# Performance work log

Hardware: AMD Instinct MI355X
Metric: run time of the kernel (lower is better)

## Reference

```python
import jax, jax.numpy as jnp
import numpy as np
from jax import lax

DIM = 1024
NUM_HEADS = 16
B, L = 4, 4096


def setup_inputs() -> dict:
    key = jax.random.key(0)
    ks = jax.random.split(key, 7)
    D = DIM // NUM_HEADS
    s = lambda fan_in: 1.0 / np.sqrt(fan_in)
    x = jax.random.normal(ks[0], (B, L, DIM), dtype=jnp.float32)
    w_qk = jax.random.uniform(ks[1], (2 * DIM, DIM), jnp.float32, -s(DIM), s(DIM))
    b_qk = jax.random.uniform(ks[2], (2 * DIM,), jnp.float32, -s(DIM), s(DIM))
    w_v = jax.random.uniform(ks[3], (DIM, DIM), jnp.float32, -s(DIM), s(DIM))
    b_v = jax.random.uniform(ks[4], (DIM,), jnp.float32, -s(DIM), s(DIM))
    # depthwise Conv1d: out_channels=D, in_channels/groups=1, kernel=3
    w_lepe = jax.random.uniform(ks[5], (D, 1, 3), jnp.float32, -s(3), s(3))
    b_lepe = jax.random.uniform(ks[6], (D,), jnp.float32, -s(3), s(3))
    return {"x": x, "w_qk": w_qk, "b_qk": b_qk, "w_v": w_v, "b_v": b_v,
            "w_lepe": w_lepe, "b_lepe": b_lepe, "num_heads": NUM_HEADS}


def _lepe_add(a, w_lepe, b_lepe):
    # a: (B,H,L,D). Faithful to torch: raw reshape (NOT transpose) to (B*H, D, L),
    # depthwise conv over last axis, reshape back to (B,H,D,L), then transpose.
    Bc, H, Lc, D = a.shape
    ar = a.reshape(Bc * H, D, Lc)
    conv = lax.conv_general_dilated(
        ar, w_lepe, window_strides=(1,), padding=((1, 1),),
        feature_group_count=D,
        dimension_numbers=("NCH", "OIH", "NCH"))
    conv = conv + b_lepe[None, :, None]
    return a + conv.reshape(Bc, H, D, Lc).transpose(0, 1, 3, 2)


def reference(x, w_qk, b_qk, w_v, b_v, w_lepe, b_lepe, num_heads):
    Bc, Lc, C = x.shape
    H = num_heads
    D = C // H
    qk = (x @ w_qk.T + b_qk).reshape(Bc, Lc, 2, H, D).transpose(2, 0, 3, 1, 4)
    q, k = qk[0], qk[1]                                  # (B,H,L,D)
    v = (x @ w_v.T + b_v).reshape(Bc, Lc, H, D).transpose(0, 2, 1, 3)
    q = jax.nn.elu(q) + 1.0
    k = jax.nn.elu(k) + 1.0
    q = _lepe_add(q, w_lepe, b_lepe)
    k = _lepe_add(k, w_lepe, b_lepe)
    k_mean = k.mean(axis=2, keepdims=True)               # (B,H,1,D)
    z = 1.0 / (jnp.einsum("bhld,bhmd->bhlm", q, k_mean) + 1e-6)  # (B,H,L,1)
    kv = jnp.einsum("bhld,bhle->bhde", k, v) / Lc        # (B,H,D,D)
    out = jnp.einsum("bhld,bhde->bhle", q, kv) * z       # (B,H,L,D)
    return out.transpose(0, 2, 1, 3).reshape(Bc, Lc, C)
```

## Files before the change

kernel.cpp:

```cpp
#include <hip/hip_runtime.h>
#include <hip/hip_bf16.h>
#include <stdint.h>

typedef __bf16 bf16;
typedef __bf16 bf16x8 __attribute__((ext_vector_type(8)));
typedef __bf16 bf16x4 __attribute__((ext_vector_type(4)));
typedef float  f32x4  __attribute__((ext_vector_type(4)));

static __device__ __forceinline__ void gll16(const void* g, void* l) {
    __builtin_amdgcn_global_load_lds((__attribute__((address_space(1))) void*)(void*)g,
                                     (__attribute__((address_space(3))) void*)l, 16, 0, 0);
}

__global__ __launch_bounds__(256) void cvt_f32_bf16(const float* __restrict__ in,
                                                    bf16* __restrict__ out, int n4) {
    int i = blockIdx.x * 256 + threadIdx.x;
    const int stride = gridDim.x * 256;
    for (; i < n4; i += stride) {
        f32x4 v = *(const f32x4*)(in + (size_t)i * 4);
        bf16x4 o;
        o[0] = (bf16)v[0]; o[1] = (bf16)v[1]; o[2] = (bf16)v[2]; o[3] = (bf16)v[3];
        *(bf16x4*)(out + (size_t)i * 4) = o;
    }
}

#define WAITV(n) asm volatile("s_waitcnt vmcnt(" #n ")" ::: "memory")
#define STA(s_, half, pass, k0_) \
    gll16(Xs + (size_t)((half) * 128 + (pass) * 64) * 1024 + (k0_), \
          lds + (s_) * 32768 + (half) * 16384 + (pass) * 8192 + t * 16)
#define STB(s_, half, pass, k0_) \
    gll16(Ws + (size_t)((half) * 128 + (pass) * 64) * 1024 + (k0_), \
          lds + 65536 + (s_) * 32768 + (half) * 16384 + (pass) * 8192 + t * 16)

__global__ __launch_bounds__(512, 2) void gemm_qkv(const bf16* __restrict__ X,
                                                   const bf16* __restrict__ W,
                                                   const float* __restrict__ b_qk,
                                                   const float* __restrict__ b_v,
                                                   bf16* __restrict__ Y) {
    __shared__ char lds[131072];
    const int t    = threadIdx.x;
    const int lane = t & 63;
    const int wid  = t >> 6;
    const int wm   = wid >> 2, wn = wid & 3;

    const int bid = blockIdx.x;
    const int wg  = (bid & 7) * 96 + (bid >> 3);
    const int m0  = (wg & 63) * 256;
    const int n0  = (wg >> 6) * 256;

    const int scol = (((t & 7) ^ ((t >> 3) & 7)) * 8);
    const bf16* Xs = X + (size_t)(m0 + (t >> 3)) * 1024 + scol;
    const bf16* Ws = W + (size_t)(n0 + (t >> 3)) * 1024 + scol;

    const int fr = lane & 15;
    const int l7 = lane & 7;
    const int ax0 = (((lane >> 4) + 0) ^ l7) << 4;
    const int ax1 = (((lane >> 4) + 4) ^ l7) << 4;
    const int baseA = wm * 16384 + fr * 128;
    const int baseB = 65536 + (wn >> 1) * 16384 + ((wn & 1) * 64 + fr) * 128;

    f32x4 acc[8][4] = {};
    bf16x8 bF[4][2];

    STB(0, 0, 0, 0); STB(0, 0, 1, 0); STB(0, 1, 0, 0); STB(0, 1, 1, 0);
    STA(0, 0, 0, 0); STA(0, 1, 0, 0); STA(0, 0, 1, 0); STA(0, 1, 1, 0);
    WAITV(2);
    __builtin_amdgcn_s_barrier();

    for (int j = 0; j < 16; ++j) {
        const int s  = j & 1;
        const int sn = s ^ 1;
        const int kn = (j + 1) << 6;
        const bool st = j < 15;
        const int sA = s * 32768 + baseA;
        const int sB = s * 32768 + baseB;

#pragma unroll
        for (int q = 0; q < 4; ++q) {
            bf16x8 aF[2][2];
#pragma unroll
            for (int m2 = 0; m2 < 2; ++m2) {
                aF[m2][0] = *(const bf16x8*)(lds + sA + (q * 2 + m2) * 2048 + ax0);
                aF[m2][1] = *(const bf16x8*)(lds + sA + (q * 2 + m2) * 2048 + ax1);
            }
            if (q == 0) {
#pragma unroll
                for (int nf = 0; nf < 4; ++nf) {
                    bF[nf][0] = *(const bf16x8*)(lds + sB + nf * 2048 + ax0);
                    bF[nf][1] = *(const bf16x8*)(lds + sB + nf * 2048 + ax1);
                }
            }
            if (st) {
                if      (q == 0) { STB(sn, 0, 0, kn); STB(sn, 0, 1, kn); }
                else if (q == 1) { STB(sn, 1, 0, kn); STB(sn, 1, 1, kn); }
                else if (q == 2) { STA(sn, 0, 0, kn); STA(sn, 1, 0, kn); }
                else             { STA(sn, 0, 1, kn); STA(sn, 1, 1, kn); }
            }
            __builtin_amdgcn_s_barrier();
            __builtin_amdgcn_s_setprio(1);
#pragma unroll
            for (int m2 = 0; m2 < 2; ++m2)
#pragma unroll
                for (int nf = 0; nf < 4; ++nf)
#pragma unroll
                    for (int kk = 0; kk < 2; ++kk)
                        acc[q * 2 + m2][nf] = __builtin_amdgcn_mfma_f32_16x16x32_bf16(
                            aF[m2][kk], bF[nf][kk], acc[q * 2 + m2][nf], 0, 0, 0);
            __builtin_amdgcn_s_setprio(0);
            if (q == 1) { if (st) { WAITV(4); } else { WAITV(0); } }
            if (q == 3 && st) { WAITV(2); }
            __builtin_amdgcn_s_barrier();
        }
    }

    const bool isqk = (n0 < 2048);
    const int crow = (lane >> 4) * 4;
#pragma unroll
    for (int nf = 0; nf < 4; ++nf) {
        const int col = n0 + wn * 64 + nf * 16 + (lane & 15);
        const float bv = isqk ? b_qk[col] : b_v[col - 2048];
#pragma unroll
        for (int mf = 0; mf < 8; ++mf) {
            const int row0 = m0 + wm * 128 + mf * 16 + crow;
#pragma unroll
            for (int jj = 0; jj < 4; ++jj) {
                float vo = acc[mf][nf][jj] + bv;
                if (isqk) vo = vo > 0.f ? vo + 1.f : expf(vo);
                Y[(size_t)(row0 + jj) * 3072 + col] = (bf16)vo;
            }
        }
    }
}
#undef STA
#undef STB
#undef WAITV

__global__ __launch_bounds__(256) void lepe(const bf16* __restrict__ Y,
                                            const float* __restrict__ wl,
                                            const float* __restrict__ bl,
                                            bf16* __restrict__ qf,
                                            bf16* __restrict__ kf) {
    const int bx = blockIdx.x;
    const int bh = bx >> 6, m = bx & 63;
    const int b = bh >> 4, h = bh & 15;
    const int isK = blockIdx.y;
    const bf16* slab = Y + (size_t)(b * 4096) * 3072 + isK * 1024 + h * 64;
    bf16* outp = (isK ? kf : qf) + (size_t)(b * 4096) * 1024 + h * 64;

    __shared__ bf16  Gs[64][72];
    __shared__ float Cs[64][65];
    __shared__ float ep[64], en[64];
    const int t = threadIdx.x;
    {
        const int d = t >> 2, c0 = (t & 3) * 16;
        const bf16* src = slab + (size_t)(d * 64 + m) * 3072 + c0;
        *(bf16x8*)&Gs[d][c0]     = *(const bf16x8*)src;
        *(bf16x8*)&Gs[d][c0 + 8] = *(const bf16x8*)(src + 8);
    }
    if (t < 64) {
        const int d = t;
        ep[d] = (m > 0)  ? (float)slab[(size_t)(d * 64 + m - 1) * 3072 + 63] : 0.f;
        en[d] = (m < 63) ? (float)slab[(size_t)(d * 64 + m + 1) * 3072 + 0]  : 0.f;
    }
    __syncthreads();
    {
        const int d = t >> 2, j0 = (t & 3) * 16;
        const float w0 = wl[d * 3], w1 = wl[d * 3 + 1], w2 = wl[d * 3 + 2], bb = bl[d];
#pragma unroll
        for (int jj = 0; jj < 16; ++jj) {
            const int j = j0 + jj;
            const float left  = (j == 0)  ? ep[d] : (float)Gs[d][j - 1];
            const float mid   = (float)Gs[d][j];
            const float right = (j == 63) ? en[d] : (float)Gs[d][j + 1];
            Cs[d][j] = w0 * left + w1 * mid + w2 * right + bb;
        }
    }
    __syncthreads();
    {
        const int j = t >> 2, c0 = (t & 3) * 16;
        const size_t l = (size_t)(m * 64 + j);
        const bf16* arow = slab + l * 3072 + c0;
        bf16* orow = outp + l * 1024 + c0;
        bf16x8 a0 = *(const bf16x8*)arow;
        bf16x8 a1 = *(const bf16x8*)(arow + 8);
        bf16x8 o0, o1;
#pragma unroll
        for (int i = 0; i < 8; ++i) {
            o0[i] = (bf16)((float)a0[i] + Cs[c0 + i][j]);
            o1[i] = (bf16)((float)a1[i] + Cs[c0 + 8 + i][j]);
        }
        *(bf16x8*)orow = o0;
        *(bf16x8*)(orow + 8) = o1;
    }
}

__global__ __launch_bounds__(256) void kv_partial(const bf16* __restrict__ kf,
                                                  const bf16* __restrict__ Y,
                                                  float* __restrict__ kvp,
                                                  float* __restrict__ ksp) {
    const int bh = blockIdx.x, ch = blockIdx.y;
    const int b = bh >> 4, h = bh & 15;
    const bf16* K = kf + (size_t)(b * 4096) * 1024 + h * 64;
    const bf16* V = Y + (size_t)(b * 4096) * 3072 + 2048 + h * 64;

    __shared__ float SM[64 * 68 * 2 + 4 * 64];
#define KS(r, c) SM[(r) * 68 + (c)]
#define VS(r, c) SM[4352 + (r) * 68 + (c)]
    float* ksr = SM + 8704;

    const int t = threadIdx.x;
    const int lane = t & 63;
    const int w = t >> 6;
    const int dg = lane >> 3, eg = lane & 7;

    f32x4 acc[8][2] = {};
    f32x4 ks0 = {}, ks1 = {};

    const int j = t >> 2, c0 = (t & 3) * 16;
    const int l0 = ch * 1024;
    const bf16* Kp = K + (size_t)(l0 + j) * 1024 + c0;
    const bf16* Vp = V + (size_t)(l0 + j) * 3072 + c0;
    bf16x8 k0 = *(const bf16x8*)Kp, k1 = *(const bf16x8*)(Kp + 8);
    bf16x8 v0 = *(const bf16x8*)Vp, v1 = *(const bf16x8*)(Vp + 8);

    for (int s = 0; s < 16; ++s) {
        __syncthreads();
        {
            f32x4 a, bx, c, d2;
#pragma unroll
            for (int i = 0; i < 4; ++i) { a[i] = (float)k0[i]; bx[i] = (float)k0[4 + i]; }
            *(f32x4*)&KS(j, c0) = a;  *(f32x4*)&KS(j, c0 + 4) = bx;
#pragma unroll
            for (int i = 0; i < 4; ++i) { c[i] = (float)k1[i]; d2[i] = (float)k1[4 + i]; }
            *(f32x4*)&KS(j, c0 + 8) = c; *(f32x4*)&KS(j, c0 + 12) = d2;
#pragma unroll
            for (int i = 0; i < 4; ++i) { a[i] = (float)v0[i]; bx[i] = (float)v0[4 + i]; }
            *(f32x4*)&VS(j, c0) = a;  *(f32x4*)&VS(j, c0 + 4) = bx;
#pragma unroll
            for (int i = 0; i < 4; ++i) { c[i] = (float)v1[i]; d2[i] = (float)v1[4 + i]; }
            *(f32x4*)&VS(j, c0 + 8) = c; *(f32x4*)&VS(j, c0 + 12) = d2;
        }
        __syncthreads();
        if (s < 15) {
            Kp += (size_t)64 * 1024; Vp += (size_t)64 * 3072;
            k0 = *(const bf16x8*)Kp; k1 = *(const bf16x8*)(Kp + 8);
            v0 = *(const bf16x8*)Vp; v1 = *(const bf16x8*)(Vp + 8);
        }
#pragma unroll
        for (int jj = 0; jj < 16; ++jj) {
            const int l = w * 16 + jj;
            f32x4 ka = *(const f32x4*)&KS(l, dg * 8);
            f32x4 kb = *(const f32x4*)&KS(l, dg * 8 + 4);
            f32x4 va = *(const f32x4*)&VS(l, eg * 8);
            f32x4 vb = *(const f32x4*)&VS(l, eg * 8 + 4);
            ks0 += ka; ks1 += kb;
#pragma unroll
            for (int i = 0; i < 4; ++i) {
                acc[i][0] += ka[i] * va;     acc[i][1] += ka[i] * vb;
                acc[4 + i][0] += kb[i] * va; acc[4 + i][1] += kb[i] * vb;
            }
        }
    }

    __syncthreads();
    if (eg == 0) {
#pragma unroll
        for (int i = 0; i < 4; ++i) {
            ksr[w * 64 + dg * 8 + i]     = ks0[i];
            ksr[w * 64 + dg * 8 + 4 + i] = ks1[i];
        }
    }
    if (w == 1 || w == 3) {
        float* buf = SM + (w >> 1) * 4352 + lane * 68;
#pragma unroll
        for (int i = 0; i < 8; ++i) {
            *(f32x4*)(buf + i * 8) = acc[i][0];
            *(f32x4*)(buf + i * 8 + 4) = acc[i][1];
        }
    }
    __syncthreads();
    if (w == 0 || w == 2) {
        float* buf = SM + (w >> 1) * 4352 + lane * 68;
#pragma unroll
        for (int i = 0; i < 8; ++i) {
            acc[i][0] += *(const f32x4*)(buf + i * 8);
            acc[i][1] += *(const f32x4*)(buf + i * 8 + 4);
        }
    }
    __syncthreads();
    if (w == 2) {
        float* buf = SM + lane * 68;
#pragma unroll
        for (int i = 0; i < 8; ++i) {
            *(f32x4*)(buf + i * 8) = acc[i][0];
            *(f32x4*)(buf + i * 8 + 4) = acc[i][1];
        }
    }
    __syncthreads();
    if (w == 0) {
        float* buf = SM + lane * 68;
#pragma unroll
        for (int i = 0; i < 8; ++i) {
            acc[i][0] += *(const f32x4*)(buf + i * 8);
            acc[i][1] += *(const f32x4*)(buf + i * 8 + 4);
        }
        float* o = kvp + (((size_t)ch * 64 + bh) * 64 + dg * 8) * 64 + eg * 8;
#pragma unroll
        for (int i = 0; i < 8; ++i) {
            *(f32x4*)(o + (size_t)i * 64)     = acc[i][0];
            *(f32x4*)(o + (size_t)i * 64 + 4) = acc[i][1];
        }
        if (eg == 0) {
#pragma unroll
            for (int i = 0; i < 8; ++i) {
                const int d = dg * 8 + i;
                ksp[(size_t)ch * 4096 + bh * 64 + d] =
                    ksr[d] + ksr[64 + d] + ksr[128 + d] + ksr[192 + d];
            }
        }
    }
#undef KS
#undef VS
}

__global__ __launch_bounds__(256) void out_kernel(const bf16* __restrict__ qf,
                                                  const float* __restrict__ kvp,
                                                  const float* __restrict__ ksp,
                                                  float* __restrict__ out) {
    const int bh = blockIdx.x;
    const int b = bh >> 4, h = bh & 15;
    __shared__ float kvS[4096];
    __shared__ float ksS[64];
    const int t = threadIdx.x;
    const float* kp = kvp + (size_t)bh * 4096;
#pragma unroll
    for (int i = 0; i < 4; ++i) {
        const int idx = i * 1024 + t * 4;
        f32x4 v = *(const f32x4*)(kp + idx);
        v = v + *(const f32x4*)(kp + 262144 + idx);
        v = v + *(const f32x4*)(kp + 524288 + idx);
        v = v + *(const f32x4*)(kp + 786432 + idx);
        *(f32x4*)(kvS + idx) = v;
    }
    if (t < 64) {
        ksS[t] = ksp[bh * 64 + t] + ksp[4096 + bh * 64 + t] +
                 ksp[8192 + bh * 64 + t] + ksp[12288 + bh * 64 + t];
    }
    __syncthreads();

    const int rg = t >> 2, eg = t & 3, e0 = eg * 16;
    const int r0 = blockIdx.y * 256 + rg * 4;
    const bf16* qbase = qf + (size_t)(b * 4096 + r0) * 1024 + h * 64;

    bf16x8 qv[4][8];
#pragma unroll
    for (int i = 0; i < 4; ++i)
#pragma unroll
        for (int s = 0; s < 8; ++s)
            qv[i][s] = *(const bf16x8*)(qbase + (size_t)i * 1024 + s * 8);

    float inv[4];
#pragma unroll
    for (int i = 0; i < 4; ++i) {
        float s = 0.f;
#pragma unroll
        for (int ss = 0; ss < 8; ++ss)
#pragma unroll
            for (int jj = 0; jj < 8; ++jj)
                s += (float)qv[i][ss][jj] * ksS[ss * 8 + jj];
        inv[i] = 1.0f / (s + 0.004096f);
    }

    f32x4 acc[4][4] = {};
#pragma unroll
    for (int d = 0; d < 64; ++d) {
        const float* kr = kvS + d * 64 + e0;
        f32x4 k0 = *(const f32x4*)kr;
        f32x4 k1 = *(const f32x4*)(kr + 4);
        f32x4 k2 = *(const f32x4*)(kr + 8);
        f32x4 k3 = *(const f32x4*)(kr + 12);
#pragma unroll
        for (int i = 0; i < 4; ++i) {
            const float qd = (float)qv[i][d >> 3][d & 7];
            acc[i][0] += qd * k0;
            acc[i][1] += qd * k1;
            acc[i][2] += qd * k2;
            acc[i][3] += qd * k3;
        }
    }
#pragma unroll
    for (int i = 0; i < 4; ++i) {
        float* orow = out + (size_t)(b * 4096 + r0 + i) * 1024 + h * 64 + e0;
#pragma unroll
        for (int q = 0; q < 4; ++q)
            *(f32x4*)(orow + q * 4) = acc[i][q] * inv[i];
    }
}

extern "C" void kernel_launch(void* const* d_in, const int* in_sizes, int n_in,
                              void* d_out, int out_size, void* d_ws, size_t ws_size,
                              hipStream_t stream) {
    const float* x      = (const float*)d_in[0];
    const float* w_qk   = (const float*)d_in[1];
    const float* b_qk   = (const float*)d_in[2];
    const float* w_v    = (const float*)d_in[3];
    const float* b_v    = (const float*)d_in[4];
    const float* w_lepe = (const float*)d_in[5];
    const float* b_lepe = (const float*)d_in[6];

    char* ws = (char*)d_ws;
    bf16*  Y   = (bf16*)ws;
    bf16*  xb  = (bf16*)(ws + 100663296);
    bf16*  Wb  = (bf16*)(ws + 134217728);
    float* kvp = (float*)(ws + 167772160);
    float* ksp = (float*)(ws + 171966464);
    bf16* qf = xb;
    bf16* kf = Wb;

    cvt_f32_bf16<<<2048, 256, 0, stream>>>(x, xb, 16777216 / 4);
    cvt_f32_bf16<<<512,  256, 0, stream>>>(w_qk, Wb, 2097152 / 4);
    cvt_f32_bf16<<<256,  256, 0, stream>>>(w_v, Wb + 2097152, 1048576 / 4);
    gemm_qkv<<<768, 512, 0, stream>>>(xb, Wb, b_qk, b_v, Y);
    lepe<<<dim3(4096, 2), 256, 0, stream>>>(Y, w_lepe, b_lepe, qf, kf);
    kv_partial<<<dim3(64, 4), 256, 0, stream>>>(kf, Y, kvp, ksp);
    out_kernel<<<dim3(64, 16), 256, 0, stream>>>(qf, kvp, ksp, (float*)d_out);
}
```

Baseline: 414.3 us.

## Fuse LePE conv into KV-partial and output kernels, drop standalone lepe pass

Removes the separate lepe kernel and computes the depthwise LePE conv inside the consumers. kv_lepe convolves each 64-row K chunk into shared memory before the KV outer product, and out_lepe builds the LePE-adjusted Q tile in shared memory before the output matmul. This avoids writing and rereading the qf/kf bf16 intermediates and one launch. The cost is extra loads, syncs and shared memory per block in kernels that have few blocks (256 and 1024), so the added latency may not be hidden.

```diff
diff --git a/kernel.cpp b/kernel.cpp
--- a/kernel.cpp
+++ b/kernel.cpp
@@ -135,78 +135,22 @@
 #undef STB
 #undef WAITV
 
-__global__ __launch_bounds__(256) void lepe(const bf16* __restrict__ Y,
-                                            const float* __restrict__ wl,
-                                            const float* __restrict__ bl,
-                                            bf16* __restrict__ qf,
-                                            bf16* __restrict__ kf) {
-    const int bx = blockIdx.x;
-    const int bh = bx >> 6, m = bx & 63;
-    const int b = bh >> 4, h = bh & 15;
-    const int isK = blockIdx.y;
-    const bf16* slab = Y + (size_t)(b * 4096) * 3072 + isK * 1024 + h * 64;
-    bf16* outp = (isK ? kf : qf) + (size_t)(b * 4096) * 1024 + h * 64;
-
-    __shared__ bf16  Gs[64][72];
-    __shared__ float Cs[64][65];
-    __shared__ float ep[64], en[64];
-    const int t = threadIdx.x;
-    {
-        const int d = t >> 2, c0 = (t & 3) * 16;
-        const bf16* src = slab + (size_t)(d * 64 + m) * 3072 + c0;
-        *(bf16x8*)&Gs[d][c0]     = *(const bf16x8*)src;
-        *(bf16x8*)&Gs[d][c0 + 8] = *(const bf16x8*)(src + 8);
-    }
-    if (t < 64) {
-        const int d = t;
-        ep[d] = (m > 0)  ? (float)slab[(size_t)(d * 64 + m - 1) * 3072 + 63] : 0.f;
-        en[d] = (m < 63) ? (float)slab[(size_t)(d * 64 + m + 1) * 3072 + 0]  : 0.f;
-    }
-    __syncthreads();
-    {
-        const int d = t >> 2, j0 = (t & 3) * 16;
-        const float w0 = wl[d * 3], w1 = wl[d * 3 + 1], w2 = wl[d * 3 + 2], bb = bl[d];
-#pragma unroll
-        for (int jj = 0; jj < 16; ++jj) {
-            const int j = j0 + jj;
-            const float left  = (j == 0)  ? ep[d] : (float)Gs[d][j - 1];
-            const float mid   = (float)Gs[d][j];
-            const float right = (j == 63) ? en[d] : (float)Gs[d][j + 1];
-            Cs[d][j] = w0 * left + w1 * mid + w2 * right + bb;
-        }
-    }
-    __syncthreads();
-    {
-        const int j = t >> 2, c0 = (t & 3) * 16;
-        const size_t l = (size_t)(m * 64 + j);
-        const bf16* arow = slab + l * 3072 + c0;
-        bf16* orow = outp + l * 1024 + c0;
-        bf16x8 a0 = *(const bf16x8*)arow;
-        bf16x8 a1 = *(const bf16x8*)(arow + 8);
-        bf16x8 o0, o1;
-#pragma unroll
-        for (int i = 0; i < 8; ++i) {
-            o0[i] = (bf16)((float)a0[i] + Cs[c0 + i][j]);
-            o1[i] = (bf16)((float)a1[i] + Cs[c0 + 8 + i][j]);
-        }
-        *(bf16x8*)orow = o0;
-        *(bf16x8*)(orow + 8) = o1;
-    }
-}
-
-__global__ __launch_bounds__(256) void kv_partial(const bf16* __restrict__ kf,
-                                                  const bf16* __restrict__ Y,
-                                                  float* __restrict__ kvp,
-                                                  float* __restrict__ ksp) {
+__global__ __launch_bounds__(256) void kv_lepe(const bf16* __restrict__ Y,
+                                               const float* __restrict__ wl,
+                                               const float* __restrict__ bl,
+                                               float* __restrict__ kvp,
+                                               float* __restrict__ ksp) {
     const int bh = blockIdx.x, ch = blockIdx.y;
     const int b = bh >> 4, h = bh & 15;
-    const bf16* K = kf + (size_t)(b * 4096) * 1024 + h * 64;
-    const bf16* V = Y + (size_t)(b * 4096) * 3072 + 2048 + h * 64;
-
-    __shared__ float SM[64 * 68 * 2 + 4 * 64];
+    const bf16* slabK = Y + (size_t)(b * 4096) * 3072 + 1024 + h * 64;
+    const bf16* Vb    = Y + (size_t)(b * 4096) * 3072 + 2048 + h * 64;
+
+    __shared__ float SM[64 * 68 * 2 + 256];
 #define KS(r, c) SM[(r) * 68 + (c)]
 #define VS(r, c) SM[4352 + (r) * 68 + (c)]
     float* ksr = SM + 8704;
+    __shared__ bf16  Gs[64][72];
+    __shared__ float ep[64], en[64];
 
     const int t = threadIdx.x;
     const int lane = t & 63;
@@ -216,36 +160,53 @@
     f32x4 acc[8][2] = {};
     f32x4 ks0 = {}, ks1 = {};
 
-    const int j = t >> 2, c0 = (t & 3) * 16;
-    const int l0 = ch * 1024;
-    const bf16* Kp = K + (size_t)(l0 + j) * 1024 + c0;
-    const bf16* Vp = V + (size_t)(l0 + j) * 3072 + c0;
-    bf16x8 k0 = *(const bf16x8*)Kp, k1 = *(const bf16x8*)(Kp + 8);
-    bf16x8 v0 = *(const bf16x8*)Vp, v1 = *(const bf16x8*)(Vp + 8);
-
-    for (int s = 0; s < 16; ++s) {
-        __syncthreads();
-        {
-            f32x4 a, bx, c, d2;
+    for (int g = 0; g < 16; ++g) {
+        const int m = ch * 16 + g;
+        __syncthreads();
+        {
+            const int d = t >> 2, c0 = (t & 3) * 16;
+            const bf16* src = slabK + (size_t)(d * 64 + m) * 3072 + c0;
+            *(bf16x8*)&Gs[d][c0]     = *(const bf16x8*)src;
+            *(bf16x8*)&Gs[d][c0 + 8] = *(const bf16x8*)(src + 8);
+        }
+        if (t < 64) {
+            ep[t] = (m > 0)  ? (float)slabK[(size_t)(t * 64 + m - 1) * 3072 + 63] : 0.f;
+            en[t] = (m < 63) ? (float)slabK[(size_t)(t * 64 + m + 1) * 3072 + 0]  : 0.f;
+        }
+        {
+            const int j = t >> 2, c0 = (t & 3) * 16;
+            const bf16* kr = slabK + (size_t)(m * 64 + j) * 3072 + c0;
+            const bf16* vr = Vb    + (size_t)(m * 64 + j) * 3072 + c0;
+            bf16x8 k0 = *(const bf16x8*)kr, k1 = *(const bf16x8*)(kr + 8);
+            bf16x8 v0 = *(const bf16x8*)vr, v1 = *(const bf16x8*)(vr + 8);
+            f32x4 a, bx;
 #pragma unroll
             for (int i = 0; i < 4; ++i) { a[i] = (float)k0[i]; bx[i] = (float)k0[4 + i]; }
             *(f32x4*)&KS(j, c0) = a;  *(f32x4*)&KS(j, c0 + 4) = bx;
 #pragma unroll
-            for (int i = 0; i < 4; ++i) { c[i] = (float)k1[i]; d2[i] = (float)k1[4 + i]; }
-            *(f32x4*)&KS(j, c0 + 8) = c; *(f32x4*)&KS(j, c0 + 12) = d2;
+            for (int i = 0; i < 4; ++i) { a[i] = (float)k1[i]; bx[i] = (float)k1[4 + i]; }
+            *(f32x4*)&KS(j, c0 + 8) = a; *(f32x4*)&KS(j, c0 + 12) = bx;
 #pragma unroll
             for (int i = 0; i < 4; ++i) { a[i] = (float)v0[i]; bx[i] = (float)v0[4 + i]; }
             *(f32x4*)&VS(j, c0) = a;  *(f32x4*)&VS(j, c0 + 4) = bx;
 #pragma unroll
-            for (int i = 0; i < 4; ++i) { c[i] = (float)v1[i]; d2[i] = (float)v1[4 + i]; }
-            *(f32x4*)&VS(j, c0 + 8) = c; *(f32x4*)&VS(j, c0 + 12) = d2;
-        }
-        __syncthreads();
-        if (s < 15) {
-            Kp += (size_t)64 * 1024; Vp += (size_t)64 * 3072;
-            k0 = *(const bf16x8*)Kp; k1 = *(const bf16x8*)(Kp + 8);
-            v0 = *(const bf16x8*)Vp; v1 = *(const bf16x8*)(Vp + 8);
-        }
+            for (int i = 0; i < 4; ++i) { a[i] = (float)v1[i]; bx[i] = (float)v1[4 + i]; }
+            *(f32x4*)&VS(j, c0 + 8) = a; *(f32x4*)&VS(j, c0 + 12) = bx;
+        }
+        __syncthreads();
+        {
+            const int d = t >> 2, j0 = (t & 3) * 16;
+            const float w0 = wl[d * 3], w1 = wl[d * 3 + 1], w2 = wl[d * 3 + 2], bb = bl[d];
+#pragma unroll
+            for (int jj = 0; jj < 16; ++jj) {
+                const int j = j0 + jj;
+                const float left  = (j == 0)  ? ep[d] : (float)Gs[d][j - 1];
+                const float mid   = (float)Gs[d][j];
+                const float right = (j == 63) ? en[d] : (float)Gs[d][j + 1];
+                KS(j, d) += w0 * left + w1 * mid + w2 * right + bb;
+            }
+        }
+        __syncthreads();
 #pragma unroll
         for (int jj = 0; jj < 16; ++jj) {
             const int l = w * 16 + jj;
@@ -323,14 +284,24 @@
 #undef VS
 }
 
-__global__ __launch_bounds__(256) void out_kernel(const bf16* __restrict__ qf,
-                                                  const float* __restrict__ kvp,
-                                                  const float* __restrict__ ksp,
-                                                  float* __restrict__ out) {
+__global__ __launch_bounds__(256) void out_lepe(const bf16* __restrict__ Y,
+                                                const float* __restrict__ wl,
+                                                const float* __restrict__ bl,
+                                                const float* __restrict__ kvp,
+                                                const float* __restrict__ ksp,
+                                                float* __restrict__ out) {
     const int bh = blockIdx.x;
+    const int ly = blockIdx.y;
     const int b = bh >> 4, h = bh & 15;
+    const bf16* slabQ = Y + (size_t)(b * 4096) * 3072 + h * 64;
+
     __shared__ float kvS[4096];
     __shared__ float ksS[64];
+    __shared__ bf16  Qs[256][72];
+    __shared__ bf16  Gs[64][72];
+    __shared__ float Cs[64][65];
+    __shared__ float ep[64], en[64];
+
     const int t = threadIdx.x;
     const float* kp = kvp + (size_t)bh * 4096;
 #pragma unroll
@@ -346,18 +317,58 @@
         ksS[t] = ksp[bh * 64 + t] + ksp[4096 + bh * 64 + t] +
                  ksp[8192 + bh * 64 + t] + ksp[12288 + bh * 64 + t];
     }
+
+    for (int g = 0; g < 4; ++g) {
+        const int m = ly * 4 + g;
+        __syncthreads();
+        {
+            const int d = t >> 2, c0 = (t & 3) * 16;
+            const bf16* src = slabQ + (size_t)(d * 64 + m) * 3072 + c0;
+            *(bf16x8*)&Gs[d][c0]     = *(const bf16x8*)src;
+            *(bf16x8*)&Gs[d][c0 + 8] = *(const bf16x8*)(src + 8);
+        }
+        if (t < 64) {
+            ep[t] = (m > 0)  ? (float)slabQ[(size_t)(t * 64 + m - 1) * 3072 + 63] : 0.f;
+            en[t] = (m < 63) ? (float)slabQ[(size_t)(t * 64 + m + 1) * 3072 + 0]  : 0.f;
+        }
+        __syncthreads();
+        {
+            const int d = t >> 2, j0 = (t & 3) * 16;
+            const float w0 = wl[d * 3], w1 = wl[d * 3 + 1], w2 = wl[d * 3 + 2], bb = bl[d];
+#pragma unroll
+            for (int jj = 0; jj < 16; ++jj) {
+                const int j = j0 + jj;
+                const float left  = (j == 0)  ? ep[d] : (float)Gs[d][j - 1];
+                const float mid   = (float)Gs[d][j];
+                const float right = (j == 63) ? en[d] : (float)Gs[d][j + 1];
+                Cs[d][j] = w0 * left + w1 * mid + w2 * right + bb;
+            }
+        }
+        __syncthreads();
+        {
+            const int j = t >> 2, c0 = (t & 3) * 16;
+            const bf16* arow = slabQ + (size_t)(m * 64 + j) * 3072 + c0;
+            bf16x8 a0 = *(const bf16x8*)arow;
+            bf16x8 a1 = *(const bf16x8*)(arow + 8);
+            bf16x8 o0, o1;
+#pragma unroll
+            for (int i = 0; i < 8; ++i) {
+                o0[i] = (bf16)((float)a0[i] + Cs[c0 + i][j]);
+                o1[i] = (bf16)((float)a1[i] + Cs[c0 + 8 + i][j]);
+            }
+            *(bf16x8*)&Qs[g * 64 + j][c0]     = o0;
+            *(bf16x8*)&Qs[g * 64 + j][c0 + 8] = o1;
+        }
+    }
     __syncthreads();
 
     const int rg = t >> 2, eg = t & 3, e0 = eg * 16;
-    const int r0 = blockIdx.y * 256 + rg * 4;
-    const bf16* qbase = qf + (size_t)(b * 4096 + r0) * 1024 + h * 64;
-
     bf16x8 qv[4][8];
 #pragma unroll
     for (int i = 0; i < 4; ++i)
 #pragma unroll
         for (int s = 0; s < 8; ++s)
-            qv[i][s] = *(const bf16x8*)(qbase + (size_t)i * 1024 + s * 8);
+            qv[i][s] = *(const bf16x8*)&Qs[rg * 4 + i][s * 8];
 
     float inv[4];
 #pragma unroll
@@ -390,7 +401,7 @@
     }
 #pragma unroll
     for (int i = 0; i < 4; ++i) {
-        float* orow = out + (size_t)(b * 4096 + r0 + i) * 1024 + h * 64 + e0;
+        float* orow = out + (size_t)(b * 4096 + ly * 256 + rg * 4 + i) * 1024 + h * 64 + e0;
 #pragma unroll
         for (int q = 0; q < 4; ++q)
             *(f32x4*)(orow + q * 4) = acc[i][q] * inv[i];
@@ -414,14 +425,11 @@
     bf16*  Wb  = (bf16*)(ws + 134217728);
     float* kvp = (float*)(ws + 167772160);
     float* ksp = (float*)(ws + 171966464);
-    bf16* qf = xb;
-    bf16* kf = Wb;
 
     cvt_f32_bf16<<<2048, 256, 0, stream>>>(x, xb, 16777216 / 4);
     cvt_f32_bf16<<<512,  256, 0, stream>>>(w_qk, Wb, 2097152 / 4);
     cvt_f32_bf16<<<256,  256, 0, stream>>>(w_v, Wb + 2097152, 1048576 / 4);
     gemm_qkv<<<768, 512, 0, stream>>>(xb, Wb, b_qk, b_v, Y);
-    lepe<<<dim3(4096, 2), 256, 0, stream>>>(Y, w_lepe, b_lepe, qf, kf);
-    kv_partial<<<dim3(64, 4), 256, 0, stream>>>(kf, Y, kvp, ksp);
-    out_kernel<<<dim3(64, 16), 256, 0, stream>>>(qf, kvp, ksp, (float*)d_out);
-}
+    kv_lepe<<<dim3(64, 4), 256, 0, stream>>>(Y, w_lepe, b_lepe, kvp, ksp);
+    out_lepe<<<dim3(64, 16), 256, 0, stream>>>(Y, w_lepe, b_lepe, kvp, ksp, (float*)d_out);
+}
```

Result: slower. 442.4 us (+6.8%).
